# Kernel tuning notes

Measured on AMD Instinct MI355X. Metric: run time of the kernel, lower is better.

## Reference

```python
import jax, jax.numpy as jnp
import numpy as np

B, S, D = 4, 4096, 1024
E, C, F = 8, 1024, 2048


def setup_inputs() -> dict:
    key = jax.random.key(0)
    ks = jax.random.split(key, 6)
    # weight init per module: uniform(-bound, bound), bound = sqrt(3)*sqrt(1/3)/sqrt(fan_in) = 1/sqrt(fan_in)
    b_d = 1.0 / np.sqrt(D)
    b_f = 1.0 / np.sqrt(F)
    return {
        "x": jax.random.normal(ks[0], (B, S, D), dtype=jnp.float32),
        "expert_weights": jax.random.uniform(ks[1], (B, E, C), dtype=jnp.float32),
        "token_indices": jax.random.randint(ks[2], (B, E, C), 0, S, dtype=jnp.int64),
        "w1": jax.random.uniform(ks[3], (E, D, F), dtype=jnp.float32, minval=-b_d, maxval=b_d),
        "w2": jax.random.uniform(ks[4], (E, D, F), dtype=jnp.float32, minval=-b_d, maxval=b_d),
        "w3": jax.random.uniform(ks[5], (E, F, D), dtype=jnp.float32, minval=-b_f, maxval=b_f),
    }


def reference(x, expert_weights, token_indices, w1, w2, w3):
    # gather: each expert picks `capacity` tokens from its batch row
    b_idx = jnp.arange(B)[:, None, None]                      # (B,1,1)
    expert_inputs = x[b_idx, token_indices]                   # (B,E,C,D)
    # grouped swiglu FFN per expert (no weight repeat needed: einsum batches over E)
    gate = jax.nn.silu(jnp.einsum('becd,edf->becf', expert_inputs, w1))
    value = jnp.einsum('becd,edf->becf', expert_inputs, w2)
    expert_outputs = jnp.einsum('becf,efd->becd', gate * value, w3)  # (B,E,C,D)
    weighted = expert_outputs * expert_weights[..., None]     # (B,E,C,D)
    # weighted scatter-add combine back to (B,S,D)
    out = jnp.zeros((B, S, D), dtype=x.dtype)
    out = out.at[b_idx, token_indices].add(weighted)
    return out
```

## Files before the change

kernel.cpp:

```cpp
#include <hip/hip_runtime.h>

#define Bn 4
#define Sn 4096
#define Dn 1024
#define En 8
#define Cn 1024
#define Fn 2048
#define Mn (Bn * Cn)

typedef __bf16 bf16x4 __attribute__((ext_vector_type(4)));
typedef __bf16 bf16x8 __attribute__((ext_vector_type(8)));
typedef float f32x4 __attribute__((ext_vector_type(4)));

#define GLOAD16(gsrc, ldst)                                                    \
  __builtin_amdgcn_global_load_lds(                                            \
      (const __attribute__((address_space(1))) void*)(gsrc),                   \
      (__attribute__((address_space(3))) void*)(ldst), 16, 0, 0)

#define VMCNT0() asm volatile("s_waitcnt vmcnt(0)" ::: "memory")

__global__ __launch_bounds__(256) void tcast_kernel(
    const float* __restrict__ in, __bf16* __restrict__ out, int K, int N) {
  __shared__ float t[32][33];
  const int e = blockIdx.z;
  const float* src = in + (size_t)e * K * N;
  __bf16* dst = out + (size_t)e * K * N;
  const int n0 = blockIdx.x << 5, k0 = blockIdx.y << 5;
  const int tx = threadIdx.x & 31, ty = threadIdx.x >> 5;
#pragma unroll
  for (int i = 0; i < 4; ++i)
    t[ty + i * 8][tx] = src[(size_t)(k0 + ty + i * 8) * N + (n0 + tx)];
  __syncthreads();
#pragma unroll
  for (int i = 0; i < 4; ++i)
    dst[(size_t)(n0 + ty + i * 8) * K + (k0 + tx)] = (__bf16)t[tx][ty + i * 8];
}

__global__ __launch_bounds__(256) void gather_cast_kernel(
    const float* __restrict__ x, const int* __restrict__ tok,
    __bf16* __restrict__ Xg) {
  const int gid = blockIdx.x * 4 + (threadIdx.x >> 6);
  const int lane = threadIdx.x & 63;
  const int e = gid >> 12, m = gid & 4095, b = m >> 10, c = m & 1023;
  const int t = tok[((size_t)b * En + e) * Cn + c];
  const float* src = x + ((size_t)b * Sn + t) * Dn;
  __bf16* dst = Xg + (size_t)gid * Dn;
#pragma unroll
  for (int i = 0; i < 4; ++i) {
    f32x4 v = *(const f32x4*)(src + i * 256 + lane * 4);
    bf16x4 o;
    o[0] = (__bf16)v[0];
    o[1] = (__bf16)v[1];
    o[2] = (__bf16)v[2];
    o[3] = (__bf16)v[3];
    *(bf16x4*)(dst + i * 256 + lane * 4) = o;
  }
}


__global__ __launch_bounds__(512, 4) void gemm12_kernel(
    const __bf16* __restrict__ Xg, const float* __restrict__ ew,
    const __bf16* __restrict__ w1T, const __bf16* __restrict__ w2T,
    __bf16* __restrict__ Hbh, int e0) {
  __shared__ __align__(16) char lds[49152];

  const int tid = threadIdx.x;
  const int lane = tid & 63, wid = tid >> 6;
  const int wr = wid >> 2, wc = wid & 3;
  const int mt = blockIdx.x, ft = blockIdx.y, eLoc = blockIdx.z;
  const int e = e0 + eLoc;

  const int srow = tid >> 2;
  const int sof = ((tid & 3) ^ ((tid >> 3) & 3)) << 3;
  const __bf16* pA = Xg + ((size_t)e * Mn + mt * 128 + srow) * Dn + sof;
  const __bf16* pB1 = w1T + ((size_t)e * Fn + ft * 128 + srow) * Dn + sof;
  const __bf16* pB2 = w2T + ((size_t)e * Fn + ft * 128 + srow) * Dn + sof;

  auto stage = [&](int slot) {
    char* d = lds + slot * 24576 + tid * 16;
    GLOAD16(pA, d);
    GLOAD16(pB1, d + 8192);
    GLOAD16(pB2, d + 16384);
    pA += 32;
    pB1 += 32;
    pB2 += 32;
  };

  const int rl = lane & 15, kb = lane >> 4;
  const int swz = (kb ^ ((rl >> 1) & 3)) << 4;

  f32x4 acc[4][4];
  const f32x4 z4 = {0.f, 0.f, 0.f, 0.f};
#pragma unroll
  for (int i = 0; i < 4; ++i)
#pragma unroll
    for (int j = 0; j < 4; ++j) acc[i][j] = z4;

  stage(0);
  VMCNT0();
  __syncthreads();

  const int KT = Dn / 32;
#pragma unroll 1
  for (int c = 0; c < KT; ++c) {
    if (c + 1 < KT) stage((c + 1) & 1);
    const char* Ab = lds + (c & 1) * 24576;
    const char* Bb = Ab + 8192;
    bf16x8 a4[4], b4[4];
#pragma unroll
    for (int f = 0; f < 4; ++f) {
      const int ra = wr * 64 + f * 16 + rl;
      a4[f] = *(const bf16x8*)(Ab + ra * 64 + swz);
      const int rb = wc * 64 + f * 16 + rl;
      b4[f] = *(const bf16x8*)(Bb + rb * 64 + swz);
    }
#pragma unroll
    for (int fm = 0; fm < 4; ++fm)
#pragma unroll
      for (int fn = 0; fn < 4; ++fn)
        acc[fm][fn] = __builtin_amdgcn_mfma_f32_16x16x32_bf16(
            a4[fm], b4[fn], acc[fm][fn], 0, 0, 0);
    __syncthreads();
  }

  const int rl0 = (lane >> 4) << 2, cl = lane & 15;
  if (wc >= 2) {
    char* reg = lds + (wr * 2 + (wc - 2)) * 8192;
#pragma unroll
    for (int fm = 0; fm < 4; ++fm)
#pragma unroll
      for (int fn = 0; fn < 4; ++fn)
#pragma unroll
        for (int j = 0; j < 4; ++j) {
          const int row = fm * 16 + rl0 + j;
          *(__bf16*)(reg + row * 128 + ((fn ^ ((row >> 2) & 3)) << 5) +
                     cl * 2) = (__bf16)acc[fm][fn][j];
        }
  }
  __syncthreads();
  if (wc < 2) {
    char* reg = lds + (wr * 2 + wc) * 8192;
    const int m0 = mt * 128 + wr * 64;
    const int b = m0 >> 10;
    const size_t ewBase = ((size_t)b * En + e) * Cn;
#pragma unroll
    for (int fm = 0; fm < 4; ++fm)
#pragma unroll
      for (int j = 0; j < 4; ++j) {
        const int row = fm * 16 + rl0 + j;
        const float wgt = ew[ewBase + ((m0 + row) & (Cn - 1))];
#pragma unroll
        for (int fn = 0; fn < 4; ++fn) {
          __bf16* p = (__bf16*)(reg + row * 128 +
                                ((fn ^ ((row >> 2) & 3)) << 5) + cl * 2);
          const float v = (float)*p;
          const float g = acc[fm][fn][j];
          *p = (__bf16)((g / (1.f + __expf(-g))) * v * wgt);
        }
      }
  }
  __syncthreads();
  __bf16* hBase = Hbh + ((size_t)eLoc * Mn + mt * 128) * Fn + ft * 128;
#pragma unroll
  for (int p = 0; p < 4; ++p) {
    const int row = p * 32 + (tid >> 4);
    const int c8 = (tid & 15) * 8;
    const int reg = (row >> 6) * 2 + (c8 >> 6);
    const int rr = row & 63, cc = c8 & 63;
    bf16x8 v = *(const bf16x8*)(lds + reg * 8192 + rr * 128 +
                                (((cc >> 4) ^ ((rr >> 2) & 3)) << 5) +
                                (cc & 15) * 2);
    *(bf16x8*)(hBase + (size_t)row * Fn + c8) = v;
  }
}

__global__ __launch_bounds__(512, 4) void gemm3_kernel(
    const __bf16* __restrict__ Hbh, const __bf16* __restrict__ w3T,
    const int* __restrict__ tok, float* __restrict__ out, int e0) {
  __shared__ __align__(16) char lds[49152];

  const int tid = threadIdx.x;
  const int lane = tid & 63, wid = tid >> 6;
  const int wr = wid >> 2, wc = wid & 3;
  const int mt = blockIdx.x, nt = blockIdx.y, eLoc = blockIdx.z;
  const int e = e0 + eLoc;

  const int srow = tid >> 2;
  const int sof = ((tid & 3) ^ ((tid >> 3) & 3)) << 3;
  const __bf16* pA = Hbh + ((size_t)eLoc * Mn + mt * 128 + srow) * Fn + sof;
  const __bf16* pB0 = w3T + ((size_t)e * Dn + nt * 256 + srow) * Fn + sof;
  const __bf16* pB1 = pB0 + (size_t)128 * Fn;

  auto stage = [&](int slot) {
    char* d = lds + slot * 24576 + tid * 16;
    GLOAD16(pA, d);
    GLOAD16(pB0, d + 8192);
    GLOAD16(pB1, d + 16384);
    pA += 32;
    pB0 += 32;
    pB1 += 32;
  };

  const int rl = lane & 15, kb = lane >> 4;
  const int swz = (kb ^ ((rl >> 1) & 3)) << 4;

  f32x4 acc[4][4];
  const f32x4 z4 = {0.f, 0.f, 0.f, 0.f};
#pragma unroll
  for (int i = 0; i < 4; ++i)
#pragma unroll
    for (int j = 0; j < 4; ++j) acc[i][j] = z4;

  stage(0);
  VMCNT0();
  __syncthreads();

  const int KT = Fn / 32;
#pragma unroll 1
  for (int c = 0; c < KT; ++c) {
    if (c + 1 < KT) stage((c + 1) & 1);
    const char* Ab = lds + (c & 1) * 24576;
    const char* Bb = Ab + 8192;
    bf16x8 a4[4], b4[4];
#pragma unroll
    for (int f = 0; f < 4; ++f) {
      const int ra = wr * 64 + f * 16 + rl;
      a4[f] = *(const bf16x8*)(Ab + ra * 64 + swz);
      const int rb = wc * 64 + f * 16 + rl;
      b4[f] = *(const bf16x8*)(Bb + rb * 64 + swz);
    }
#pragma unroll
    for (int fm = 0; fm < 4; ++fm)
#pragma unroll
      for (int fn = 0; fn < 4; ++fn)
        acc[fm][fn] = __builtin_amdgcn_mfma_f32_16x16x32_bf16(
            a4[fm], b4[fn], acc[fm][fn], 0, 0, 0);
    __syncthreads();
  }

  const int m0 = mt * 128 + wr * 64;
  const int b = m0 >> 10;
  const int rl0 = (lane >> 4) << 2, cl = lane & 15;
  const int colBase = nt * 256 + wc * 64 + cl;
#pragma unroll
  for (int fm = 0; fm < 4; ++fm) {
#pragma unroll
    for (int j = 0; j < 4; ++j) {
      const int m = m0 + fm * 16 + rl0 + j;
      const int c2 = m & (Cn - 1);
      const int t = tok[((size_t)b * En + e) * Cn + c2];
      float* orow = out + ((size_t)b * Sn + t) * Dn + colBase;
#pragma unroll
      for (int fn = 0; fn < 4; ++fn)
        atomicAdd(orow + fn * 16, acc[fm][fn][j]);
    }
  }
}

extern "C" void kernel_launch(void* const* d_in, const int* in_sizes, int n_in,
                              void* d_out, int out_size, void* d_ws,
                              size_t ws_size, hipStream_t stream) {
  const float* x = (const float*)d_in[0];
  const float* ew = (const float*)d_in[1];
  const int* tok = (const int*)d_in[2];
  const float* w1 = (const float*)d_in[3];
  const float* w2 = (const float*)d_in[4];
  const float* w3 = (const float*)d_in[5];
  float* out = (float*)d_out;

  const size_t wE = (size_t)En * Dn * Fn;
  const size_t xgE = (size_t)En * Mn * Dn;
  const size_t hbE = (size_t)(En / 2) * Mn * Fn;
  __bf16* w1T = (__bf16*)d_ws;
  __bf16* w2T = w1T + wE;
  __bf16* w3T = w2T + wE;
  __bf16* Xg = w3T + wE;
  __bf16* Hbh = Xg + xgE;
  const size_t need = (3 * wE + xgE + hbE) * sizeof(__bf16);
  if (ws_size < need) return;

  (void)hipMemsetAsync(d_out, 0, (size_t)Bn * Sn * Dn * sizeof(float), stream);

  tcast_kernel<<<dim3(Fn / 32, Dn / 32, En), 256, 0, stream>>>(w1, w1T, Dn, Fn);
  tcast_kernel<<<dim3(Fn / 32, Dn / 32, En), 256, 0, stream>>>(w2, w2T, Dn, Fn);
  tcast_kernel<<<dim3(Dn / 32, Fn / 32, En), 256, 0, stream>>>(w3, w3T, Fn, Dn);
  gather_cast_kernel<<<dim3(En * Mn / 4), 256, 0, stream>>>(x, tok, Xg);
  for (int h = 0; h < 2; ++h) {
    gemm12_kernel<<<dim3(32, 16, En / 2), 512, 0, stream>>>(Xg, ew, w1T, w2T,
                                                            Hbh, h * (En / 2));
    gemm3_kernel<<<dim3(32, 4, En / 2), 512, 0, stream>>>(Hbh, w3T, tok, out,
                                                          h * (En / 2));
  }
}
```

Baseline: 678.0 us.

## Triple-buffer GEMM K-loops with one barrier per step and restructure the SwiGLU epilogue

Both GEMM kernels move from double to triple LDS buffering. The prefetch for step c+2 is issued after the current fragments are read, and waits are partial (vmcnt(3)) with a single barrier per step plus raised wave priority around the MFMA block. Occupancy hints drop from 4 to 2 blocks to fit the larger LDS footprint. In gemm12 each wave now accumulates both the gate and value tiles in registers, so the LDS exchange before SiLU*value is removed. However, wave columns 2-3 recompute the same tiles as columns 0-1, which doubles MFMA work in that kernel.

Result: slower. 1.194 ms (+76.1%).

```diff
diff --git a/kernel.cpp b/kernel.cpp
--- a/kernel.cpp
+++ b/kernel.cpp
@@ -17,7 +17,11 @@
       (const __attribute__((address_space(1))) void*)(gsrc),                   \
       (__attribute__((address_space(3))) void*)(ldst), 16, 0, 0)
 
+#define VMCNT3() asm volatile("s_waitcnt vmcnt(3)" ::: "memory")
 #define VMCNT0() asm volatile("s_waitcnt vmcnt(0)" ::: "memory")
+#define SCHEDB() __builtin_amdgcn_sched_barrier(0)
+#define SBAR() __builtin_amdgcn_s_barrier()
+#define PRIO(p) __builtin_amdgcn_s_setprio(p)
 
 __global__ __launch_bounds__(256) void tcast_kernel(
     const float* __restrict__ in, __bf16* __restrict__ out, int K, int N) {
@@ -58,11 +62,11 @@
 }
 
 
-__global__ __launch_bounds__(512, 4) void gemm12_kernel(
+__global__ __launch_bounds__(512, 2) void gemm12_kernel(
     const __bf16* __restrict__ Xg, const float* __restrict__ ew,
     const __bf16* __restrict__ w1T, const __bf16* __restrict__ w2T,
     __bf16* __restrict__ Hbh, int e0) {
-  __shared__ __align__(16) char lds[49152];
+  __shared__ __align__(16) char lds[73728];
 
   const int tid = threadIdx.x;
   const int lane = tid & 63, wid = tid >> 6;
@@ -89,73 +93,79 @@
   const int rl = lane & 15, kb = lane >> 4;
   const int swz = (kb ^ ((rl >> 1) & 3)) << 4;
 
-  f32x4 acc[4][4];
+  f32x4 acc1[4][4], acc2[4][4];
   const f32x4 z4 = {0.f, 0.f, 0.f, 0.f};
 #pragma unroll
   for (int i = 0; i < 4; ++i)
 #pragma unroll
-    for (int j = 0; j < 4; ++j) acc[i][j] = z4;
+    for (int j = 0; j < 4; ++j) {
+      acc1[i][j] = z4;
+      acc2[i][j] = z4;
+    }
 
   stage(0);
-  VMCNT0();
-  __syncthreads();
+  stage(1);
 
   const int KT = Dn / 32;
 #pragma unroll 1
   for (int c = 0; c < KT; ++c) {
-    if (c + 1 < KT) stage((c + 1) & 1);
-    const char* Ab = lds + (c & 1) * 24576;
-    const char* Bb = Ab + 8192;
-    bf16x8 a4[4], b4[4];
+    if (c + 2 < KT) VMCNT3();
+    else VMCNT0();
+    SBAR();
+    SCHEDB();
+    const char* Ab = lds + (c % 3) * 24576;
+    const char* B1b = Ab + 8192;
+    const char* B2b = Ab + 16384;
+    bf16x8 a4[4], b14[4], b24[4];
 #pragma unroll
     for (int f = 0; f < 4; ++f) {
       const int ra = wr * 64 + f * 16 + rl;
       a4[f] = *(const bf16x8*)(Ab + ra * 64 + swz);
+      const int rb = wc * 32 + f * 8 + (rl & 7);
+      (void)rb;
+    }
+#pragma unroll
+    for (int f = 0; f < 4; ++f) {
       const int rb = wc * 64 + f * 16 + rl;
-      b4[f] = *(const bf16x8*)(Bb + rb * 64 + swz);
-    }
+      b14[f] = *(const bf16x8*)(B1b + ((rb & 127)) * 64 + swz);
+      b24[f] = *(const bf16x8*)(B2b + ((rb & 127)) * 64 + swz);
+    }
+    if (c + 2 < KT) stage((c + 2) % 3);
+    PRIO(1);
 #pragma unroll
     for (int fm = 0; fm < 4; ++fm)
 #pragma unroll
-      for (int fn = 0; fn < 4; ++fn)
-        acc[fm][fn] = __builtin_amdgcn_mfma_f32_16x16x32_bf16(
-            a4[fm], b4[fn], acc[fm][fn], 0, 0, 0);
-    __syncthreads();
-  }
+      for (int fn = 0; fn < 4; ++fn) {
+        acc1[fm][fn] = __builtin_amdgcn_mfma_f32_16x16x32_bf16(
+            a4[fm], b14[fn], acc1[fm][fn], 0, 0, 0);
+        acc2[fm][fn] = __builtin_amdgcn_mfma_f32_16x16x32_bf16(
+            a4[fm], b24[fn], acc2[fm][fn], 0, 0, 0);
+      }
+    PRIO(0);
+  }
+  __syncthreads();
 
   const int rl0 = (lane >> 4) << 2, cl = lane & 15;
-  if (wc >= 2) {
-    char* reg = lds + (wr * 2 + (wc - 2)) * 8192;
-#pragma unroll
-    for (int fm = 0; fm < 4; ++fm)
-#pragma unroll
-      for (int fn = 0; fn < 4; ++fn)
-#pragma unroll
-        for (int j = 0; j < 4; ++j) {
-          const int row = fm * 16 + rl0 + j;
-          *(__bf16*)(reg + row * 128 + ((fn ^ ((row >> 2) & 3)) << 5) +
-                     cl * 2) = (__bf16)acc[fm][fn][j];
-        }
-  }
-  __syncthreads();
-  if (wc < 2) {
-    char* reg = lds + (wr * 2 + wc) * 8192;
+  char* reg = lds + ((wr * 2 + (wc & 1)) * 8192) + ((wc >> 1) * 4096);
+  {
     const int m0 = mt * 128 + wr * 64;
     const int b = m0 >> 10;
     const size_t ewBase = ((size_t)b * En + e) * Cn;
-#pragma unroll
-    for (int fm = 0; fm < 4; ++fm)
+    const int fmBase = (wc >> 1) * 2;
+#pragma unroll
+    for (int fm = 0; fm < 2; ++fm)
 #pragma unroll
       for (int j = 0; j < 4; ++j) {
-        const int row = fm * 16 + rl0 + j;
+        const int row = (fmBase + fm) * 16 + rl0 + j;
         const float wgt = ew[ewBase + ((m0 + row) & (Cn - 1))];
 #pragma unroll
         for (int fn = 0; fn < 4; ++fn) {
-          __bf16* p = (__bf16*)(reg + row * 128 +
-                                ((fn ^ ((row >> 2) & 3)) << 5) + cl * 2);
-          const float v = (float)*p;
-          const float g = acc[fm][fn][j];
-          *p = (__bf16)((g / (1.f + __expf(-g))) * v * wgt);
+          const float g = acc1[fmBase + fm][fn][j];
+          const float v = acc2[fmBase + fm][fn][j];
+          const float h = (g / (1.f + __expf(-g))) * v * wgt;
+          const int lrow = row - fmBase * 16;
+          *(__bf16*)(reg + lrow * 128 + ((fn ^ ((row >> 2) & 3)) << 5) +
+                     cl * 2) = (__bf16)h;
         }
       }
   }
@@ -165,19 +175,20 @@
   for (int p = 0; p < 4; ++p) {
     const int row = p * 32 + (tid >> 4);
     const int c8 = (tid & 15) * 8;
-    const int reg = (row >> 6) * 2 + (c8 >> 6);
-    const int rr = row & 63, cc = c8 & 63;
-    bf16x8 v = *(const bf16x8*)(lds + reg * 8192 + rr * 128 +
+    const int rr = row & 63, ccq = c8 >> 6;
+    const char* rgn = lds + (((row >> 6) * 2 + ccq) * 8192);
+    const int cc = c8 & 63;
+    bf16x8 v = *(const bf16x8*)(rgn + (rr >> 5) * 4096 + (rr & 31) * 128 +
                                 (((cc >> 4) ^ ((rr >> 2) & 3)) << 5) +
                                 (cc & 15) * 2);
     *(bf16x8*)(hBase + (size_t)row * Fn + c8) = v;
   }
 }
 
-__global__ __launch_bounds__(512, 4) void gemm3_kernel(
+__global__ __launch_bounds__(512, 2) void gemm3_kernel(
     const __bf16* __restrict__ Hbh, const __bf16* __restrict__ w3T,
     const int* __restrict__ tok, float* __restrict__ out, int e0) {
-  __shared__ __align__(16) char lds[49152];
+  __shared__ __align__(16) char lds[73728];
 
   const int tid = threadIdx.x;
   const int lane = tid & 63, wid = tid >> 6;
@@ -212,14 +223,16 @@
     for (int j = 0; j < 4; ++j) acc[i][j] = z4;
 
   stage(0);
-  VMCNT0();
-  __syncthreads();
+  stage(1);
 
   const int KT = Fn / 32;
 #pragma unroll 1
   for (int c = 0; c < KT; ++c) {
-    if (c + 1 < KT) stage((c + 1) & 1);
-    const char* Ab = lds + (c & 1) * 24576;
+    if (c + 2 < KT) VMCNT3();
+    else VMCNT0();
+    SBAR();
+    SCHEDB();
+    const char* Ab = lds + (c % 3) * 24576;
     const char* Bb = Ab + 8192;
     bf16x8 a4[4], b4[4];
 #pragma unroll
@@ -229,13 +242,15 @@
       const int rb = wc * 64 + f * 16 + rl;
       b4[f] = *(const bf16x8*)(Bb + rb * 64 + swz);
     }
+    if (c + 2 < KT) stage((c + 2) % 3);
+    PRIO(1);
 #pragma unroll
     for (int fm = 0; fm < 4; ++fm)
 #pragma unroll
       for (int fn = 0; fn < 4; ++fn)
         acc[fm][fn] = __builtin_amdgcn_mfma_f32_16x16x32_bf16(
             a4[fm], b4[fn], acc[fm][fn], 0, 0, 0);
-    __syncthreads();
+    PRIO(0);
   }
 
   const int m0 = mt * 128 + wr * 64;
```

## Triple-buffer LDS in both GEMMs with prefetch distance two and one barrier

Applied to the files above, without the earlier changes.

Both GEMM main loops move from double to triple LDS buffering. Each iteration issues the async global-to-LDS loads for stage c+2, waits only on stage c with a partial vmcnt, and uses a single barrier per iteration instead of a full drain plus a trailing __syncthreads. MFMA sections are wrapped in s_setprio so waves doing math get scheduling priority. The aim is to hide global load latency behind more compute. The cost is LDS per block rising from 48KB to 72KB, which can reduce how many blocks fit on a CU.

New measurement: 653.6 us. -3.6%, faster.

```diff
diff --git a/kernel.cpp b/kernel.cpp
--- a/kernel.cpp
+++ b/kernel.cpp
@@ -17,7 +17,11 @@
       (const __attribute__((address_space(1))) void*)(gsrc),                   \
       (__attribute__((address_space(3))) void*)(ldst), 16, 0, 0)
 
+#define VMCNT3() asm volatile("s_waitcnt vmcnt(3)" ::: "memory")
 #define VMCNT0() asm volatile("s_waitcnt vmcnt(0)" ::: "memory")
+#define SCHEDB() __builtin_amdgcn_sched_barrier(0)
+#define SBAR() __builtin_amdgcn_s_barrier()
+#define PRIO(p) __builtin_amdgcn_s_setprio(p)
 
 __global__ __launch_bounds__(256) void tcast_kernel(
     const float* __restrict__ in, __bf16* __restrict__ out, int K, int N) {
@@ -62,7 +66,7 @@
     const __bf16* __restrict__ Xg, const float* __restrict__ ew,
     const __bf16* __restrict__ w1T, const __bf16* __restrict__ w2T,
     __bf16* __restrict__ Hbh, int e0) {
-  __shared__ __align__(16) char lds[49152];
+  __shared__ __align__(16) char lds[73728];
 
   const int tid = threadIdx.x;
   const int lane = tid & 63, wid = tid >> 6;
@@ -97,14 +101,16 @@
     for (int j = 0; j < 4; ++j) acc[i][j] = z4;
 
   stage(0);
-  VMCNT0();
-  __syncthreads();
+  stage(1);
 
   const int KT = Dn / 32;
 #pragma unroll 1
   for (int c = 0; c < KT; ++c) {
-    if (c + 1 < KT) stage((c + 1) & 1);
-    const char* Ab = lds + (c & 1) * 24576;
+    if (c < KT - 1) VMCNT3();
+    else VMCNT0();
+    SBAR();
+    SCHEDB();
+    const char* Ab = lds + (c % 3) * 24576;
     const char* Bb = Ab + 8192;
     bf16x8 a4[4], b4[4];
 #pragma unroll
@@ -114,14 +120,17 @@
       const int rb = wc * 64 + f * 16 + rl;
       b4[f] = *(const bf16x8*)(Bb + rb * 64 + swz);
     }
+    if (c + 2 < KT) stage((c + 2) % 3);
+    PRIO(1);
 #pragma unroll
     for (int fm = 0; fm < 4; ++fm)
 #pragma unroll
       for (int fn = 0; fn < 4; ++fn)
         acc[fm][fn] = __builtin_amdgcn_mfma_f32_16x16x32_bf16(
             a4[fm], b4[fn], acc[fm][fn], 0, 0, 0);
-    __syncthreads();
-  }
+    PRIO(0);
+  }
+  __syncthreads();
 
   const int rl0 = (lane >> 4) << 2, cl = lane & 15;
   if (wc >= 2) {
@@ -177,7 +186,7 @@
 __global__ __launch_bounds__(512, 4) void gemm3_kernel(
     const __bf16* __restrict__ Hbh, const __bf16* __restrict__ w3T,
     const int* __restrict__ tok, float* __restrict__ out, int e0) {
-  __shared__ __align__(16) char lds[49152];
+  __shared__ __align__(16) char lds[73728];
 
   const int tid = threadIdx.x;
   const int lane = tid & 63, wid = tid >> 6;
@@ -212,14 +221,16 @@
     for (int j = 0; j < 4; ++j) acc[i][j] = z4;
 
   stage(0);
-  VMCNT0();
-  __syncthreads();
+  stage(1);
 
   const int KT = Fn / 32;
 #pragma unroll 1
   for (int c = 0; c < KT; ++c) {
-    if (c + 1 < KT) stage((c + 1) & 1);
-    const char* Ab = lds + (c & 1) * 24576;
+    if (c < KT - 1) VMCNT3();
+    else VMCNT0();
+    SBAR();
+    SCHEDB();
+    const char* Ab = lds + (c % 3) * 24576;
     const char* Bb = Ab + 8192;
     bf16x8 a4[4], b4[4];
 #pragma unroll
@@ -229,13 +240,15 @@
       const int rb = wc * 64 + f * 16 + rl;
       b4[f] = *(const bf16x8*)(Bb + rb * 64 + swz);
     }
+    if (c + 2 < KT) stage((c + 2) % 3);
+    PRIO(1);
 #pragma unroll
     for (int fm = 0; fm < 4; ++fm)
 #pragma unroll
       for (int fn = 0; fn < 4; ++fn)
         acc[fm][fn] = __builtin_amdgcn_mfma_f32_16x16x32_bf16(
             a4[fm], b4[fn], acc[fm][fn], 0, 0, 0);
-    __syncthreads();
+    PRIO(0);
   }
 
   const int m0 = mt * 128 + wr * 64;
```
